# Kernel optimization log

Measured on AMD Instinct MI355X. Metric: run time of the kernel, lower is better.

## Reference

```python
import jax, jax.numpy as jnp
import numpy as np

P_ASEM = 0.8
IN_SIZE = 128


def setup_inputs() -> dict:
    key = jax.random.key(0)
    k1, k2, k3, k4 = jax.random.split(key, 4)
    B, N, D = 8, 2048, IN_SIZE
    x = jax.random.normal(k1, (B, N, D), dtype=jnp.float32)
    adj = jax.random.uniform(k2, (B, N, N), dtype=jnp.float32)
    # Linear(2D -> 1): weight [1, 2D], bias [1] (torch convention). Store as vector/scalar.
    bound = 1.0 / np.sqrt(2 * D)
    W = jax.random.uniform(k3, (2 * D,), minval=-bound, maxval=bound, dtype=jnp.float32)
    b = jax.random.uniform(k4, (), minval=-bound, maxval=bound, dtype=jnp.float32)
    return {"x": x, "adj": adj, "W": W, "b": b}


def reference(x, adj, W, b):
    # linear(cat(xi, xj)) == x @ W[:D] (row term) + x @ W[D:] (col term) + b
    # This avoids materializing the [B, N, N, 2D] concat tensor.
    D = x.shape[-1]
    si = jnp.einsum('bnd,d->bn', x, W[:D])  # contribution of xi (varies over axis -2)
    sj = jnp.einsum('bnd,d->bn', x, W[D:])  # contribution of xj (varies over axis -1)
    scores = si[:, :, None] + sj[:, None, :] + b  # [B, N, N]
    return P_ASEM * jax.nn.sigmoid(scores) + (1.0 - P_ASEM) * adj
```

## Files before the change

kernel.cpp:

```cpp
#include <hip/hip_runtime.h>

#define BSZ   8
#define NN    2048
#define DD    128
#define NROWS (BSZ * NN)
#define N4    (NN / 4)
#define P_A   0.8f
#define P_B   0.2f

typedef float v4f __attribute__((ext_vector_type(4)));

__global__ __launch_bounds__(256) void row_dots(const float* __restrict__ x,
                                                const float* __restrict__ W,
                                                const float* __restrict__ bias,
                                                float* __restrict__ si,
                                                float* __restrict__ sj) {
    int gtid = blockIdx.x * blockDim.x + threadIdx.x;
    int wave = gtid >> 6;
    int lane = threadIdx.x & 63;
    int row0 = wave * 2;
    if (row0 >= NROWS) return;

    const float2* xr0 = (const float2*)(x + (size_t)row0 * DD);
    const float2* xr1 = (const float2*)(x + (size_t)(row0 + 1) * DD);
    const float2* W2  = (const float2*)W;

    float2 wi = W2[lane];
    float2 wj = W2[lane + 64];
    float2 a0 = xr0[lane];
    float2 a1 = xr1[lane];

    float si0 = a0.x * wi.x + a0.y * wi.y;
    float sj0 = a0.x * wj.x + a0.y * wj.y;
    float si1 = a1.x * wi.x + a1.y * wi.y;
    float sj1 = a1.x * wj.x + a1.y * wj.y;

    #pragma unroll
    for (int off = 32; off > 0; off >>= 1) {
        si0 += __shfl_down(si0, off, 64);
        sj0 += __shfl_down(sj0, off, 64);
        si1 += __shfl_down(si1, off, 64);
        sj1 += __shfl_down(sj1, off, 64);
    }
    if (lane == 0) {
        float bb = bias[0];
        si[row0]     = si0 + bb;
        si[row0 + 1] = si1 + bb;
        sj[row0]     = sj0;
        sj[row0 + 1] = sj1;
    }
}

__global__ __launch_bounds__(256) void fuse_kernel(const v4f* __restrict__ adj,
                                                   const float* __restrict__ si,
                                                   const v4f* __restrict__ sj,
                                                   v4f* __restrict__ out) {
    const int tid = threadIdx.x;

    #pragma unroll 2
    for (int r = 0; r < 8; ++r) {
        const int row = blockIdx.x * 8 + r;
        const int b   = row >> 11;
        const float s = si[row];
        const v4f* sjrow = sj + (b << 9);
        const size_t base = (size_t)row * N4;

        v4f sv0 = sjrow[tid];
        v4f sv1 = sjrow[tid + 256];
        v4f av0 = __builtin_nontemporal_load(adj + base + tid);
        v4f av1 = __builtin_nontemporal_load(adj + base + tid + 256);

        v4f o0, o1;
        o0.x = P_A * __builtin_amdgcn_rcpf(1.0f + __expf(-(s + sv0.x))) + P_B * av0.x;
        o0.y = P_A * __builtin_amdgcn_rcpf(1.0f + __expf(-(s + sv0.y))) + P_B * av0.y;
        o0.z = P_A * __builtin_amdgcn_rcpf(1.0f + __expf(-(s + sv0.z))) + P_B * av0.z;
        o0.w = P_A * __builtin_amdgcn_rcpf(1.0f + __expf(-(s + sv0.w))) + P_B * av0.w;
        o1.x = P_A * __builtin_amdgcn_rcpf(1.0f + __expf(-(s + sv1.x))) + P_B * av1.x;
        o1.y = P_A * __builtin_amdgcn_rcpf(1.0f + __expf(-(s + sv1.y))) + P_B * av1.y;
        o1.z = P_A * __builtin_amdgcn_rcpf(1.0f + __expf(-(s + sv1.z))) + P_B * av1.z;
        o1.w = P_A * __builtin_amdgcn_rcpf(1.0f + __expf(-(s + sv1.w))) + P_B * av1.w;

        __builtin_nontemporal_store(o0, out + base + tid);
        __builtin_nontemporal_store(o1, out + base + tid + 256);
    }
}

extern "C" void kernel_launch(void* const* d_in, const int* in_sizes, int n_in,
                              void* d_out, int out_size, void* d_ws, size_t ws_size,
                              hipStream_t stream) {
    const float* x    = (const float*)d_in[0];
    const float* adj  = (const float*)d_in[1];
    const float* W    = (const float*)d_in[2];
    const float* bias = (const float*)d_in[3];

    float* si = (float*)d_ws;
    float* sj = si + NROWS;

    row_dots<<<NROWS / 8, 256, 0, stream>>>(x, W, bias, si, sj);

    fuse_kernel<<<NROWS / 8, 256, 0, stream>>>(
        (const v4f*)adj, si, (const v4f*)sj, (v4f*)d_out);
}
```

Baseline: 236.6 us.

## Fuse row-dot and sigmoid-blend kernels into one cooperative launch with grid sync

Merges the row-dot kernel and the elementwise blend kernel into a single cooperative kernel of 1024 blocks, each handling 16 rows, with a grid-wide barrier between the phases. This removes a kernel launch and the gap between launches. Each block now loads the sj vector once and reuses it across its 16 rows. The cost is a grid barrier, a requirement that all blocks be co-resident, and fewer, larger blocks for the bandwidth-bound streaming phase.

```diff
diff --git a/kernel.cpp b/kernel.cpp
--- a/kernel.cpp
+++ b/kernel.cpp
@@ -1,4 +1,7 @@
 #include <hip/hip_runtime.h>
+#include <hip/hip_cooperative_groups.h>
+
+namespace cg = cooperative_groups;
 
 #define BSZ   8
 #define NN    2048
@@ -8,80 +11,85 @@
 #define P_A   0.8f
 #define P_B   0.2f
 
+#define BLOCKS 1024
+#define RPB    16
+
 typedef float v4f __attribute__((ext_vector_type(4)));
 
-__global__ __launch_bounds__(256) void row_dots(const float* __restrict__ x,
-                                                const float* __restrict__ W,
-                                                const float* __restrict__ bias,
-                                                float* __restrict__ si,
-                                                float* __restrict__ sj) {
-    int gtid = blockIdx.x * blockDim.x + threadIdx.x;
-    int wave = gtid >> 6;
-    int lane = threadIdx.x & 63;
-    int row0 = wave * 2;
-    if (row0 >= NROWS) return;
+__global__ __launch_bounds__(256, 4) void fused_all(const float* __restrict__ x,
+                                                    const v4f*  __restrict__ adj,
+                                                    const float* __restrict__ W,
+                                                    const float* __restrict__ bias,
+                                                    float* __restrict__ si,
+                                                    float* __restrict__ sj,
+                                                    v4f* __restrict__ out) {
+    const int tid  = threadIdx.x;
+    const int lane = tid & 63;
+    const int wave = tid >> 6;
+    const int row0 = blockIdx.x * RPB;
 
-    const float2* xr0 = (const float2*)(x + (size_t)row0 * DD);
-    const float2* xr1 = (const float2*)(x + (size_t)(row0 + 1) * DD);
-    const float2* W2  = (const float2*)W;
+    {
+        const float2* W2 = (const float2*)W;
+        const float2 wi = W2[lane];
+        const float2 wj = W2[lane + 64];
 
-    float2 wi = W2[lane];
-    float2 wj = W2[lane + 64];
-    float2 a0 = xr0[lane];
-    float2 a1 = xr1[lane];
+        const int r0 = row0 + wave * 4;
+        float a_si[4], a_sj[4];
+        #pragma unroll
+        for (int k = 0; k < 4; ++k) {
+            const float2* xr = (const float2*)(x + (size_t)(r0 + k) * DD);
+            float2 a = xr[lane];
+            a_si[k] = a.x * wi.x + a.y * wi.y;
+            a_sj[k] = a.x * wj.x + a.y * wj.y;
+        }
+        #pragma unroll
+        for (int off = 32; off > 0; off >>= 1) {
+            #pragma unroll
+            for (int k = 0; k < 4; ++k) {
+                a_si[k] += __shfl_down(a_si[k], off, 64);
+                a_sj[k] += __shfl_down(a_sj[k], off, 64);
+            }
+        }
+        if (lane == 0) {
+            float bb = bias[0];
+            #pragma unroll
+            for (int k = 0; k < 4; ++k) {
+                si[r0 + k] = a_si[k] + bb;
+                sj[r0 + k] = a_sj[k];
+            }
+        }
+    }
 
-    float si0 = a0.x * wi.x + a0.y * wi.y;
-    float sj0 = a0.x * wj.x + a0.y * wj.y;
-    float si1 = a1.x * wi.x + a1.y * wi.y;
-    float sj1 = a1.x * wj.x + a1.y * wj.y;
+    cg::this_grid().sync();
 
-    #pragma unroll
-    for (int off = 32; off > 0; off >>= 1) {
-        si0 += __shfl_down(si0, off, 64);
-        sj0 += __shfl_down(sj0, off, 64);
-        si1 += __shfl_down(si1, off, 64);
-        sj1 += __shfl_down(sj1, off, 64);
-    }
-    if (lane == 0) {
-        float bb = bias[0];
-        si[row0]     = si0 + bb;
-        si[row0 + 1] = si1 + bb;
-        sj[row0]     = sj0;
-        sj[row0 + 1] = sj1;
-    }
-}
+    {
+        const int b = row0 >> 11;
+        const v4f* sjrow = (const v4f*)(sj + (b << 11));
+        const v4f sv0 = sjrow[tid];
+        const v4f sv1 = sjrow[tid + 256];
 
-__global__ __launch_bounds__(256) void fuse_kernel(const v4f* __restrict__ adj,
-                                                   const float* __restrict__ si,
-                                                   const v4f* __restrict__ sj,
-                                                   v4f* __restrict__ out) {
-    const int tid = threadIdx.x;
+        #pragma unroll 4
+        for (int r = 0; r < RPB; ++r) {
+            const int row = row0 + r;
+            const float s = si[row];
+            const size_t base = (size_t)row * N4;
 
-    #pragma unroll 2
-    for (int r = 0; r < 8; ++r) {
-        const int row = blockIdx.x * 8 + r;
-        const int b   = row >> 11;
-        const float s = si[row];
-        const v4f* sjrow = sj + (b << 9);
-        const size_t base = (size_t)row * N4;
+            v4f av0 = __builtin_nontemporal_load(adj + base + tid);
+            v4f av1 = __builtin_nontemporal_load(adj + base + tid + 256);
 
-        v4f sv0 = sjrow[tid];
-        v4f sv1 = sjrow[tid + 256];
-        v4f av0 = __builtin_nontemporal_load(adj + base + tid);
-        v4f av1 = __builtin_nontemporal_load(adj + base + tid + 256);
+            v4f o0, o1;
+            o0.x = P_A * __builtin_amdgcn_rcpf(1.0f + __expf(-(s + sv0.x))) + P_B * av0.x;
+            o0.y = P_A * __builtin_amdgcn_rcpf(1.0f + __expf(-(s + sv0.y))) + P_B * av0.y;
+            o0.z = P_A * __builtin_amdgcn_rcpf(1.0f + __expf(-(s + sv0.z))) + P_B * av0.z;
+            o0.w = P_A * __builtin_amdgcn_rcpf(1.0f + __expf(-(s + sv0.w))) + P_B * av0.w;
+            o1.x = P_A * __builtin_amdgcn_rcpf(1.0f + __expf(-(s + sv1.x))) + P_B * av1.x;
+            o1.y = P_A * __builtin_amdgcn_rcpf(1.0f + __expf(-(s + sv1.y))) + P_B * av1.y;
+            o1.z = P_A * __builtin_amdgcn_rcpf(1.0f + __expf(-(s + sv1.z))) + P_B * av1.z;
+            o1.w = P_A * __builtin_amdgcn_rcpf(1.0f + __expf(-(s + sv1.w))) + P_B * av1.w;
 
-        v4f o0, o1;
-        o0.x = P_A * __builtin_amdgcn_rcpf(1.0f + __expf(-(s + sv0.x))) + P_B * av0.x;
-        o0.y = P_A * __builtin_amdgcn_rcpf(1.0f + __expf(-(s + sv0.y))) + P_B * av0.y;
-        o0.z = P_A * __builtin_amdgcn_rcpf(1.0f + __expf(-(s + sv0.z))) + P_B * av0.z;
-        o0.w = P_A * __builtin_amdgcn_rcpf(1.0f + __expf(-(s + sv0.w))) + P_B * av0.w;
-        o1.x = P_A * __builtin_amdgcn_rcpf(1.0f + __expf(-(s + sv1.x))) + P_B * av1.x;
-        o1.y = P_A * __builtin_amdgcn_rcpf(1.0f + __expf(-(s + sv1.y))) + P_B * av1.y;
-        o1.z = P_A * __builtin_amdgcn_rcpf(1.0f + __expf(-(s + sv1.z))) + P_B * av1.z;
-        o1.w = P_A * __builtin_amdgcn_rcpf(1.0f + __expf(-(s + sv1.w))) + P_B * av1.w;
-
-        __builtin_nontemporal_store(o0, out + base + tid);
-        __builtin_nontemporal_store(o1, out + base + tid + 256);
+            __builtin_nontemporal_store(o0, out + base + tid);
+            __builtin_nontemporal_store(o1, out + base + tid + 256);
+        }
     }
 }
 
@@ -95,9 +103,11 @@
 
     float* si = (float*)d_ws;
     float* sj = si + NROWS;
+    v4f*   out = (v4f*)d_out;
+    const v4f* adjv = (const v4f*)adj;
 
-    row_dots<<<NROWS / 8, 256, 0, stream>>>(x, W, bias, si, sj);
-
-    fuse_kernel<<<NROWS / 8, 256, 0, stream>>>(
-        (const v4f*)adj, si, (const v4f*)sj, (v4f*)d_out);
+    void* args[] = {(void*)&x, (void*)&adjv, (void*)&W, (void*)&bias,
+                    (void*)&si, (void*)&sj, (void*)&out};
+    hipLaunchCooperativeKernel((void*)fused_all, dim3(BLOCKS), dim3(256),
+                               args, 0, stream);
 }
```

After: 300.0 us. 26.8% more time.
